# Optimization experiments

Measured on AMD Instinct MI355X. Metric: run time of the kernel, lower is better.

## Reference

```python
import jax, jax.numpy as jnp
import numpy as np

S, B, D_MODEL, H, DH = 2048, 2, 1024, 16, 64
FACTOR = 1.0 / np.sqrt(DH).astype(np.float32)


def setup_inputs() -> dict:
    key = jax.random.key(0)
    ks = jax.random.split(key, 12)
    sc = 0.02
    inp = {
        'query': jax.random.normal(ks[0], (S, B, D_MODEL), jnp.float32),
        'key': jax.random.normal(ks[1], (S, B, D_MODEL), jnp.float32),
        'value': jax.random.normal(ks[2], (S, B, D_MODEL), jnp.float32),
        # causal mask [seq_q, seq_k, 1]; 0 -> masked
        'mask': jnp.tril(jnp.ones((S, S), dtype=bool))[:, :, None],
        'Wq': jax.random.normal(ks[3], (H * DH, D_MODEL), jnp.float32) * sc,
        'bq': jnp.zeros((H * DH,), jnp.float32),
        'Wk': jax.random.normal(ks[4], (H * DH, D_MODEL), jnp.float32) * sc,
        'bk': jnp.zeros((H * DH,), jnp.float32),
        'Wv': jax.random.normal(ks[5], (H * DH, D_MODEL), jnp.float32) * sc,
        'bv': jnp.zeros((H * DH,), jnp.float32),
        'Wo': jax.random.normal(ks[6], (D_MODEL, H * DH), jnp.float32) * sc,
        'bo': jnp.zeros((D_MODEL,), jnp.float32),
    }
    return inp


def _split_heads(x):
    # pattern: 's b (head_dim head_num) -> s b head_num head_dim' (head_dim is OUTER)
    s, b, _ = x.shape
    return x.reshape(s, b, DH, H).transpose(0, 1, 3, 2)  # [s,b,H,DH]


def reference(query, key, value, mask, Wq, bq, Wk, bk, Wv, bv, Wo, bo):
    q = _split_heads(query @ Wq.T + bq)
    k = _split_heads(key @ Wk.T + bk)
    v = _split_heads(value @ Wv.T + bv)
    scores = jnp.einsum('ibhd,jbhd->ijbh', q, k) * FACTOR  # [i,j,b,h]
    scores = jnp.where(mask[..., None], scores, -jnp.inf)
    attn = jax.nn.softmax(scores, axis=1)  # softmax over keys (dim=1)
    out = jnp.einsum('ijbh,jbhd->ibhd', attn, v)  # [i,b,h,d]
    out = out.reshape(S, B, H * DH)  # 'i b h d -> i b (h d)'
    return out @ Wo.T + bo
```

## Files before the change

kernel.cpp:

```cpp
#include <hip/hip_runtime.h>


typedef float f32x4 __attribute__((ext_vector_type(4)));
typedef float f32x16 __attribute__((ext_vector_type(16)));
typedef __bf16 bf16x8_t __attribute__((ext_vector_type(8)));
typedef unsigned short ushort8 __attribute__((ext_vector_type(8)));
typedef unsigned int uint4v __attribute__((ext_vector_type(4)));
typedef unsigned int uint2v __attribute__((ext_vector_type(2)));

#define S_LEN 2048
#define BATCH 2
#define DMODEL 1024
#define NHEAD 16
#define DHEAD 64
#define K_SCALE 0.18033688011112042f

__device__ __forceinline__ unsigned short f2bf(float x) {
  unsigned int u = __builtin_bit_cast(unsigned int, x);
  u += 0x7fffu + ((u >> 16) & 1u);
  return (unsigned short)(u >> 16);
}

__device__ __forceinline__ f32x4 mfma16(ushort8 a, ushort8 b, f32x4 c) {
  return __builtin_amdgcn_mfma_f32_16x16x32_bf16(
      __builtin_bit_cast(bf16x8_t, a), __builtin_bit_cast(bf16x8_t, b), c, 0, 0, 0);
}
__device__ __forceinline__ f32x16 mfma32(ushort8 a, ushort8 b, f32x16 c) {
  return __builtin_amdgcn_mfma_f32_32x32x16_bf16(
      __builtin_bit_cast(bf16x8_t, a), __builtin_bit_cast(bf16x8_t, b), c, 0, 0, 0);
}

__device__ __forceinline__ ushort8 pack8(float4 a, float4 b, float s) {
  ushort8 t;
  t[0] = f2bf(a.x * s); t[1] = f2bf(a.y * s); t[2] = f2bf(a.z * s); t[3] = f2bf(a.w * s);
  t[4] = f2bf(b.x * s); t[5] = f2bf(b.y * s); t[6] = f2bf(b.z * s); t[7] = f2bf(b.w * s);
  return t;
}

__device__ __forceinline__ void gload16(unsigned short* lds, const unsigned short* g) {
  __builtin_amdgcn_global_load_lds(
      (const __attribute__((address_space(1))) unsigned int*)g,
      (__attribute__((address_space(3))) unsigned int*)lds, 16, 0, 0);
}

__global__ __launch_bounds__(256) void cvt_kernel(
    const float* __restrict__ q, const float* __restrict__ k, const float* __restrict__ v,
    const float* __restrict__ wq, const float* __restrict__ wk,
    const float* __restrict__ wv, const float* __restrict__ wo,
    unsigned short* __restrict__ qB, unsigned short* __restrict__ kB,
    unsigned short* __restrict__ vB, unsigned short* __restrict__ wqB,
    unsigned short* __restrict__ wkB, unsigned short* __restrict__ wvB,
    unsigned short* __restrict__ woB)
{
  const int c = blockIdx.x * 256 + threadIdx.x;
  const float* s; unsigned short* d; int base;
  if      (c < 524288)  { s = q;  d = qB;  base = 0; }
  else if (c < 1048576) { s = k;  d = kB;  base = 524288; }
  else if (c < 1572864) { s = v;  d = vB;  base = 1048576; }
  else if (c < 1703936) { s = wq; d = wqB; base = 1572864; }
  else if (c < 1835008) { s = wk; d = wkB; base = 1703936; }
  else if (c < 1966080) { s = wv; d = wvB; base = 1835008; }
  else                  { s = wo; d = woB; base = 1966080; }
  const size_t off = (size_t)(c - base) * 8;
  const float4 v0 = *reinterpret_cast<const float4*>(s + off);
  const float4 v1 = *reinterpret_cast<const float4*>(s + off + 4);
  *reinterpret_cast<ushort8*>(d + off) = pack8(v0, v1, 1.0f);
}

template<bool OUTBF16>
__global__ __launch_bounds__(256) void gemm_bf16_kernel(
    const unsigned short* __restrict__ A, const unsigned short* __restrict__ W,
    const float* __restrict__ bias, void* __restrict__ Cv, float oscale)
{
  __shared__ __align__(16) unsigned short As[2][128 * 64];
  __shared__ __align__(16) unsigned short Ws[2][64 * 64];
  const int tid = threadIdx.x;
  const int lane = tid & 63;
  const int w = tid >> 6;
  const int wm = (w >> 1) * 64, wn = (w & 1) * 32;
  const int g = lane >> 4, lr = lane & 15;

  const int bid = (int)blockIdx.x;
  const int widx = (bid & 7) * 64 + (bid >> 3);
  const int n0 = (widx & 15) * 64;
  const int m0 = (widx >> 4) * 128;

  f32x4 acc[4][2] = {};

#define STAGE(buf, k0)                                                              \
  {                                                                                 \
    _Pragma("unroll")                                                               \
    for (int ii = 0; ii < 4; ++ii) {                                                \
      const int c = ii * 256 + tid;                                                 \
      const int row = c >> 3;                                                       \
      const int sl = (c & 7) ^ (row & 7);                                           \
      gload16(&As[buf][c * 8], A + (size_t)(m0 + row) * DMODEL + (k0) + sl * 8);    \
    }                                                                               \
    _Pragma("unroll")                                                               \
    for (int ii = 0; ii < 2; ++ii) {                                                \
      const int c = ii * 256 + tid;                                                 \
      const int row = c >> 3;                                                       \
      const int sl = (c & 7) ^ (row & 7);                                           \
      gload16(&Ws[buf][c * 8], W + (size_t)(n0 + row) * DMODEL + (k0) + sl * 8);    \
    }                                                                               \
  }

  STAGE(0, 0);
  int cur = 0;

  for (int t = 0; t < 16; ++t) {
    __syncthreads();
    if (t < 15) STAGE(cur ^ 1, (t + 1) * 64);

    const char* ab = (const char*)&As[cur][0];
    const char* wb = (const char*)&Ws[cur][0];
#pragma unroll
    for (int kk = 0; kk < 2; ++kk) {
      ushort8 af[4], bw[2];
#pragma unroll
      for (int mt = 0; mt < 4; ++mt) {
        const int row = wm + mt * 16 + lr;
        af[mt] = *reinterpret_cast<const ushort8*>(
            ab + row * 128 + (((kk * 4 + g) ^ (row & 7)) << 4));
      }
#pragma unroll
      for (int nt = 0; nt < 2; ++nt) {
        const int row = wn + nt * 16 + lr;
        bw[nt] = *reinterpret_cast<const ushort8*>(
            wb + row * 128 + (((kk * 4 + g) ^ (row & 7)) << 4));
      }
      __builtin_amdgcn_s_setprio(1);
#pragma unroll
      for (int mt = 0; mt < 4; ++mt)
#pragma unroll
        for (int nt = 0; nt < 2; ++nt)
          acc[mt][nt] = mfma16(af[mt], bw[nt], acc[mt][nt]);
      __builtin_amdgcn_s_setprio(0);
    }
    cur ^= 1;
  }
#undef STAGE

#pragma unroll
  for (int nt = 0; nt < 2; ++nt) {
    const int col = n0 + wn + nt * 16 + lr;
    const float bv = bias[col];
#pragma unroll
    for (int mt = 0; mt < 4; ++mt)
#pragma unroll
      for (int r = 0; r < 4; ++r) {
        const int rowg = m0 + wm + mt * 16 + g * 4 + r;
        const float vv = (acc[mt][nt][r] + bv) * oscale;
        if constexpr (OUTBF16)
          ((unsigned short*)Cv)[(size_t)rowg * DMODEL + col] = f2bf(vv);
        else
          ((float*)Cv)[(size_t)rowg * DMODEL + col] = vv;
      }
  }
}

__global__ __launch_bounds__(256) void head_tr0_kernel(
    const unsigned short* __restrict__ in, unsigned short* __restrict__ out)
{
  __shared__ __align__(16) unsigned short T[32 * 256];
  const int tid = threadIdx.x;
  const int n0 = blockIdx.x * 32, o0 = blockIdx.y * 256;
#pragma unroll
  for (int i = 0; i < 4; ++i) {
    const int c = i * 256 + tid;
    const int row = c >> 5, c8 = c & 31;
    ushort8 v = *reinterpret_cast<const ushort8*>(in + (size_t)(n0 + row) * DMODEL + o0 + c8 * 8);
    int y = (row * 512 + c8 * 16) ^ ((row & 3) << 5);
    *reinterpret_cast<ushort8*>((char*)T + y) = v;
  }
  __syncthreads();
  const int d0 = o0 >> 4, s0 = n0 >> 1;
#pragma unroll
  for (int rep = 0; rep < 2; ++rep) {
    const int e = rep * 256 + tid;
    const int hh = e & 15, s = (e >> 4) & 15, b = (e >> 8) & 1;
    const int n = s * 2 + b;
    unsigned short vals[16];
#pragma unroll
    for (int dd = 0; dd < 16; ++dd) {
      int y = n * 512 + ((dd * 32 + hh * 2) ^ ((n & 3) << 5));
      vals[dd] = *(const unsigned short*)((const char*)T + y);
    }
    uint4v w0, w1;
#pragma unroll
    for (int j = 0; j < 4; ++j) {
      w0[j] = (unsigned)vals[2 * j] | ((unsigned)vals[2 * j + 1] << 16);
      w1[j] = (unsigned)vals[8 + 2 * j] | ((unsigned)vals[8 + 2 * j + 1] << 16);
    }
    unsigned short* dst = out + ((size_t)(b * 16 + hh) * S_LEN + s0 + s) * DHEAD + d0;
    *reinterpret_cast<uint4v*>(dst) = w0;
    *reinterpret_cast<uint4v*>(dst + 8) = w1;
  }
}

__global__ __launch_bounds__(256) void head_tr1_kernel(
    const unsigned short* __restrict__ in, unsigned short* __restrict__ out)
{
  __shared__ __align__(16) unsigned short T[64 * 64];
  const int tid = threadIdx.x;
  const int n0 = blockIdx.x * 64, o0 = blockIdx.y * 64;
#pragma unroll
  for (int i = 0; i < 2; ++i) {
    const int c = i * 256 + tid;
    const int row = c >> 3, c8 = c & 7;
    ushort8 v = *reinterpret_cast<const ushort8*>(in + (size_t)(n0 + row) * DMODEL + o0 + c8 * 8);
    int y = (row * 128 + c8 * 16) ^ ((row & 7) << 4);
    *reinterpret_cast<ushort8*>((char*)T + y) = v;
  }
  __syncthreads();
  const int d0 = o0 >> 4, s0 = n0 >> 1;
  const int shalf = tid & 1, seg = tid >> 1;
  const int dd = seg & 3, hh = (seg >> 2) & 15, b = (seg >> 6) & 1;
  unsigned short vals[16];
#pragma unroll
  for (int i = 0; i < 16; ++i) {
    const int s = shalf * 16 + i;
    const int n = s * 2 + b;
    int y = n * 128 + (((dd * 16 + hh) * 2) ^ ((n & 7) << 4));
    vals[i] = *(const unsigned short*)((const char*)T + y);
  }
  uint4v w0, w1;
#pragma unroll
  for (int j = 0; j < 4; ++j) {
    w0[j] = (unsigned)vals[2 * j] | ((unsigned)vals[2 * j + 1] << 16);
    w1[j] = (unsigned)vals[8 + 2 * j] | ((unsigned)vals[8 + 2 * j + 1] << 16);
  }
  unsigned short* dst = out + ((size_t)(b * 16 + hh) * DHEAD + d0 + dd) * S_LEN + s0 + shalf * 16;
  *reinterpret_cast<uint4v*>(dst) = w0;
  *reinterpret_cast<uint4v*>(dst + 8) = w1;
}

__global__ __launch_bounds__(256, 2) void attn_kernel(
    const unsigned short* __restrict__ Qh, const unsigned short* __restrict__ Kh,
    const unsigned short* __restrict__ Vh, unsigned short* __restrict__ O)
{
  __shared__ __align__(16) unsigned short Ks[2][64 * 64];
  __shared__ __align__(16) unsigned short Vs[2][64 * 64];

  const int tid = threadIdx.x;
  const int lane = tid & 63;
  const int w = tid >> 6;
  const int ln31 = lane & 31;
  const int hf = lane >> 5;

  const int bx = blockIdx.x;
  const int hb = bx & 31;
  const int head = hb & 15, b = hb >> 4;
  const int i = bx >> 5;
  const int qt = (i < 8) ? (15 - i) : (i - 8);
  const int q0 = qt * 128;
  const size_t hoff = (size_t)(b * NHEAD + head) * (S_LEN * DHEAD);
  const unsigned short* Qg = Qh + hoff;
  const unsigned short* Kg = Kh + hoff;
  const unsigned short* Vg = Vh + hoff;

  ushort8 qf[4];
  {
    const int qrow = q0 + w * 32 + ln31;
#pragma unroll
    for (int kt = 0; kt < 4; ++kt)
      qf[kt] = *reinterpret_cast<const ushort8*>(Qg + (size_t)qrow * DHEAD + kt * 16 + hf * 8);
  }

  f32x16 oa0 = {0}, oa1 = {0};
  float mrun = -1e30f, ssum = 0.f;

  const int nkt = 2 * qt + 2;
  const int qg = q0 + w * 32 + ln31;
  const int qw_max = q0 + w * 32 + 31;

  ushort8 sK0, sK1, sV0, sV1;
  const int r0 = tid >> 3, f0 = tid & 7;
  const int r1 = r0 + 32, f1 = f0;

#define LOAD_TILES(kv)                                                            \
  {                                                                               \
    sK0 = *reinterpret_cast<const ushort8*>(Kg + (size_t)((kv) + r0) * 64 + f0 * 8); \
    sK1 = *reinterpret_cast<const ushort8*>(Kg + (size_t)((kv) + r1) * 64 + f1 * 8); \
    sV0 = *reinterpret_cast<const ushort8*>(Vg + (size_t)r0 * S_LEN + (kv) + f0 * 8); \
    sV1 = *reinterpret_cast<const ushort8*>(Vg + (size_t)r1 * S_LEN + (kv) + f1 * 8); \
  }
#define WRITE_TILES(buf)                                                          \
  {                                                                               \
    *reinterpret_cast<ushort8*>((char*)&Ks[buf][0] + ((r0 * 128 + f0 * 16) ^ ((r0 & 7) << 4))) = sK0; \
    *reinterpret_cast<ushort8*>((char*)&Ks[buf][0] + ((r1 * 128 + f1 * 16) ^ ((r1 & 7) << 4))) = sK1; \
    *reinterpret_cast<ushort8*>((char*)&Vs[buf][0] + ((r0 * 128 + f0 * 16) ^ ((r0 & 7) << 4))) = sV0; \
    *reinterpret_cast<ushort8*>((char*)&Vs[buf][0] + ((r1 * 128 + f1 * 16) ^ ((r1 & 7) << 4))) = sV1; \
  }

  LOAD_TILES(0);
  WRITE_TILES(0);
  __syncthreads();
  int cur = 0;

  const int kb0 = ln31 * 128 + ((hf * 16) ^ ((ln31 & 7) << 4));
  const int kb1 = (32 + ln31) * 128 + ((hf * 16) ^ (((32 + ln31) & 7) << 4));

  for (int t = 0; t < nkt; ++t) {
    const int kv0 = t * 64;
    const bool has_next = (t + 1) < nkt;
    if (has_next) LOAD_TILES(kv0 + 64);

    if (kv0 <= qw_max) {
      f32x16 sc0 = {0}, sc1 = {0};
      {
        const char* ksb = (const char*)&Ks[cur][0];
        __builtin_amdgcn_s_setprio(1);
#pragma unroll
        for (int kt = 0; kt < 4; ++kt) {
          ushort8 kf0 = *reinterpret_cast<const ushort8*>(ksb + (kb0 ^ (kt << 5)));
          ushort8 kf1 = *reinterpret_cast<const ushort8*>(ksb + (kb1 ^ (kt << 5)));
          sc0 = mfma32(kf0, qf[kt], sc0);
          sc1 = mfma32(kf1, qf[kt], sc1);
        }
        __builtin_amdgcn_s_setprio(0);
      }

      if (has_next) WRITE_TILES(cur ^ 1);

      if (kv0 + 63 > q0 + w * 32) {
#pragma unroll
        for (int r = 0; r < 16; ++r) {
          const int keyb = kv0 + (r & 3) + 8 * (r >> 2) + 4 * hf;
          if (keyb > qg) sc0[r] = -1e30f;
          if (keyb + 32 > qg) sc1[r] = -1e30f;
        }
      }

      float pmax = sc0[0];
#pragma unroll
      for (int r = 1; r < 16; ++r) pmax = fmaxf(pmax, sc0[r]);
#pragma unroll
      for (int r = 0; r < 16; ++r) pmax = fmaxf(pmax, sc1[r]);
      pmax = fmaxf(pmax, __shfl_xor(pmax, 32, 64));

      if (!__all(pmax <= mrun + 8.0f)) {
        const float mnew = fmaxf(mrun, pmax);
        const float scl = exp2f(mrun - mnew);
        ssum *= scl;
#pragma unroll
        for (int r = 0; r < 16; ++r) { oa0[r] *= scl; oa1[r] *= scl; }
        mrun = mnew;
      }

      float pv0[16], pv1[16];
      float psum = 0.f;
#pragma unroll
      for (int r = 0; r < 16; ++r) {
        pv0[r] = exp2f(sc0[r] - mrun);
        pv1[r] = exp2f(sc1[r] - mrun);
        psum += pv0[r] + pv1[r];
      }
      psum += __shfl_xor(psum, 32, 64);
      ssum += psum;

      unsigned int cc[16], pc[16];
#pragma unroll
      for (int j = 0; j < 8; ++j) {
        asm("v_cvt_pk_bf16_f32 %0, %1, %2" : "=v"(cc[j]) : "v"(pv0[2 * j]), "v"(pv0[2 * j + 1]));
        asm("v_cvt_pk_bf16_f32 %0, %1, %2" : "=v"(cc[8 + j]) : "v"(pv1[2 * j]), "v"(pv1[2 * j + 1]));
      }
#pragma unroll
      for (int j = 0; j < 16; ++j)
        pc[j] = (unsigned int)__shfl_xor((int)cc[j], 32, 64);

      uint4v pfw[4];
#pragma unroll
      for (int mt = 0; mt < 2; ++mt) {
#pragma unroll
        for (int ktl = 0; ktl < 2; ++ktl) {
          const int o = mt * 8 + ktl * 4;
          uint4v u;
          u[0] = hf ? pc[o + 2] : cc[o + 0];
          u[1] = hf ? pc[o + 3] : cc[o + 1];
          u[2] = hf ? cc[o + 2] : pc[o + 0];
          u[3] = hf ? cc[o + 3] : pc[o + 1];
          pfw[mt * 2 + ktl] = u;
        }
      }

      {
        const char* vsb = (const char*)&Vs[cur][0];
        __builtin_amdgcn_s_setprio(1);
#pragma unroll
        for (int kt = 0; kt < 4; ++kt) {
          ushort8 vf0 = *reinterpret_cast<const ushort8*>(vsb + (kb0 ^ (kt << 5)));
          ushort8 vf1 = *reinterpret_cast<const ushort8*>(vsb + (kb1 ^ (kt << 5)));
          ushort8 pfr = __builtin_bit_cast(ushort8, pfw[kt]);
          oa0 = mfma32(vf0, pfr, oa0);
          oa1 = mfma32(vf1, pfr, oa1);
        }
        __builtin_amdgcn_s_setprio(0);
      }
    } else {
      if (has_next) WRITE_TILES(cur ^ 1);
    }

    __syncthreads();
    cur ^= 1;
  }

  const float inv = 1.0f / ssum;
  unsigned short* ob = O + ((size_t)qg * BATCH + b) * DMODEL + head * DHEAD;
#pragma unroll
  for (int mt2 = 0; mt2 < 2; ++mt2) {
#pragma unroll
    for (int rq = 0; rq < 4; ++rq) {
      const int dd = mt2 * 32 + 8 * rq + 4 * hf;
      const f32x16& a = mt2 ? oa1 : oa0;
      unsigned int w0, w1;
      asm("v_cvt_pk_bf16_f32 %0, %1, %2" : "=v"(w0)
          : "v"(a[4 * rq + 0] * inv), "v"(a[4 * rq + 1] * inv));
      asm("v_cvt_pk_bf16_f32 %0, %1, %2" : "=v"(w1)
          : "v"(a[4 * rq + 2] * inv), "v"(a[4 * rq + 3] * inv));
      uint2v pk = { w0, w1 };
      *reinterpret_cast<uint2v*>(ob + dd) = pk;
    }
  }
#undef LOAD_TILES
#undef WRITE_TILES
}

extern "C" void kernel_launch(void* const* d_in, const int* in_sizes, int n_in,
                              void* d_out, int out_size, void* d_ws, size_t ws_size,
                              hipStream_t stream)
{
  (void)in_sizes; (void)n_in; (void)out_size; (void)ws_size;
  const float* query = (const float*)d_in[0];
  const float* key_  = (const float*)d_in[1];
  const float* value = (const float*)d_in[2];
  const float* Wq = (const float*)d_in[4];
  const float* bq = (const float*)d_in[5];
  const float* Wk = (const float*)d_in[6];
  const float* bk = (const float*)d_in[7];
  const float* Wv = (const float*)d_in[8];
  const float* bv = (const float*)d_in[9];
  const float* Wo = (const float*)d_in[10];
  const float* bo = (const float*)d_in[11];
  float* out = (float*)d_out;

  const size_t NE = (size_t)4096 * DMODEL;
  const size_t NW = (size_t)DMODEL * DMODEL;
  unsigned short* qB  = (unsigned short*)d_ws;
  unsigned short* kB  = qB + NE;
  unsigned short* vB  = kB + NE;
  unsigned short* g1  = vB + NE;
  unsigned short* Qh  = g1 + NE;
  unsigned short* Kh  = Qh + NE;
  unsigned short* Vh  = Kh + NE;
  unsigned short* wqB = Vh + NE;
  unsigned short* wkB = wqB + NW;
  unsigned short* wvB = wkB + NW;
  unsigned short* woB = wvB + NW;
  unsigned short* aO  = qB;

  dim3 t0grid(128, 4);
  dim3 t1grid(64, 16);

  cvt_kernel<<<dim3(8192), 256, 0, stream>>>(query, key_, value, Wq, Wk, Wv, Wo,
                                             qB, kB, vB, wqB, wkB, wvB, woB);
  gemm_bf16_kernel<true><<<dim3(512), 256, 0, stream>>>(qB, wqB, bq, g1, 1.0f);
  head_tr0_kernel<<<t0grid, 256, 0, stream>>>(g1, Qh);
  gemm_bf16_kernel<true><<<dim3(512), 256, 0, stream>>>(kB, wkB, bk, g1, K_SCALE);
  head_tr0_kernel<<<t0grid, 256, 0, stream>>>(g1, Kh);
  gemm_bf16_kernel<true><<<dim3(512), 256, 0, stream>>>(vB, wvB, bv, g1, 1.0f);
  head_tr1_kernel<<<t1grid, 256, 0, stream>>>(g1, Vh);
  attn_kernel<<<dim3(512), 256, 0, stream>>>(Qh, Kh, Vh, aO);
  gemm_bf16_kernel<false><<<dim3(512), 256, 0, stream>>>(aO, woB, bo, out, 1.0f);
}
```

Baseline: 155.1 us.

## Use direct global-to-LDS async loads with 64-row query tiles in attention

The attention kernel now runs 1024 blocks of 128 threads, each owning 64 query rows, in place of 512 blocks of 256 threads owning 128 rows. Launch bounds change to allow three blocks per CU. K/V staging switches from register round-trips to direct global-to-LDS loads (gload16), with the XOR swizzle applied to the source addresses. The loop is reordered so the barrier sits first and the next tile is prefetched before compute. Masking is limited to the last tile, and the per-warp causal skip branch is gone. The intent is finer causal load balance and better overlap of loads with MFMA work. The cost is that K/V tiles are fetched twice as often per query row.

```diff
diff --git a/kernel.cpp b/kernel.cpp
--- a/kernel.cpp
+++ b/kernel.cpp
@@ -235,7 +235,7 @@
   *reinterpret_cast<uint4v*>(dst + 8) = w1;
 }
 
-__global__ __launch_bounds__(256, 2) void attn_kernel(
+__global__ __launch_bounds__(128, 3) void attn_kernel(
     const unsigned short* __restrict__ Qh, const unsigned short* __restrict__ Kh,
     const unsigned short* __restrict__ Vh, unsigned short* __restrict__ O)
 {
@@ -251,9 +251,9 @@
   const int bx = blockIdx.x;
   const int hb = bx & 31;
   const int head = hb & 15, b = hb >> 4;
-  const int i = bx >> 5;
-  const int qt = (i < 8) ? (15 - i) : (i - 8);
-  const int q0 = qt * 128;
+  const int qt = 31 - (bx >> 5);
+  const int q0 = qt * 64;
+  const int nkt = qt + 1;
   const size_t hoff = (size_t)(b * NHEAD + head) * (S_LEN * DHEAD);
   const unsigned short* Qg = Qh + hoff;
   const unsigned short* Kg = Kh + hoff;
@@ -269,141 +269,129 @@
 
   f32x16 oa0 = {0}, oa1 = {0};
   float mrun = -1e30f, ssum = 0.f;
-
-  const int nkt = 2 * qt + 2;
   const int qg = q0 + w * 32 + ln31;
-  const int qw_max = q0 + w * 32 + 31;
-
-  ushort8 sK0, sK1, sV0, sV1;
-  const int r0 = tid >> 3, f0 = tid & 7;
-  const int r1 = r0 + 32, f1 = f0;
-
-#define LOAD_TILES(kv)                                                            \
-  {                                                                               \
-    sK0 = *reinterpret_cast<const ushort8*>(Kg + (size_t)((kv) + r0) * 64 + f0 * 8); \
-    sK1 = *reinterpret_cast<const ushort8*>(Kg + (size_t)((kv) + r1) * 64 + f1 * 8); \
-    sV0 = *reinterpret_cast<const ushort8*>(Vg + (size_t)r0 * S_LEN + (kv) + f0 * 8); \
-    sV1 = *reinterpret_cast<const ushort8*>(Vg + (size_t)r1 * S_LEN + (kv) + f1 * 8); \
-  }
-#define WRITE_TILES(buf)                                                          \
-  {                                                                               \
-    *reinterpret_cast<ushort8*>((char*)&Ks[buf][0] + ((r0 * 128 + f0 * 16) ^ ((r0 & 7) << 4))) = sK0; \
-    *reinterpret_cast<ushort8*>((char*)&Ks[buf][0] + ((r1 * 128 + f1 * 16) ^ ((r1 & 7) << 4))) = sK1; \
-    *reinterpret_cast<ushort8*>((char*)&Vs[buf][0] + ((r0 * 128 + f0 * 16) ^ ((r0 & 7) << 4))) = sV0; \
-    *reinterpret_cast<ushort8*>((char*)&Vs[buf][0] + ((r1 * 128 + f1 * 16) ^ ((r1 & 7) << 4))) = sV1; \
-  }
-
-  LOAD_TILES(0);
-  WRITE_TILES(0);
-  __syncthreads();
+
+#define STAGE(buf, kv)                                                             \
+  {                                                                                \
+    _Pragma("unroll")                                                              \
+    for (int ii = 0; ii < 4; ++ii) {                                               \
+      const int c = ii * 128 + tid;                                                \
+      const int row = c >> 3;                                                      \
+      const int sl = (c & 7) ^ (row & 7);                                          \
+      gload16(&Ks[buf][c * 8], Kg + (size_t)((kv) + row) * 64 + sl * 8);           \
+    }                                                                              \
+    _Pragma("unroll")                                                              \
+    for (int ii = 0; ii < 4; ++ii) {                                               \
+      const int c = ii * 128 + tid;                                                \
+      const int row = c >> 3;                                                      \
+      const int sl = (c & 7) ^ (row & 7);                                          \
+      gload16(&Vs[buf][c * 8], Vg + (size_t)row * S_LEN + (kv) + sl * 8);          \
+    }                                                                              \
+  }
+
+  STAGE(0, 0);
   int cur = 0;
 
   const int kb0 = ln31 * 128 + ((hf * 16) ^ ((ln31 & 7) << 4));
-  const int kb1 = (32 + ln31) * 128 + ((hf * 16) ^ (((32 + ln31) & 7) << 4));
+  const int kb1 = (32 + ln31) * 128 + ((hf * 16) ^ ((ln31 & 7) << 4));
 
   for (int t = 0; t < nkt; ++t) {
     const int kv0 = t * 64;
-    const bool has_next = (t + 1) < nkt;
-    if (has_next) LOAD_TILES(kv0 + 64);
-
-    if (kv0 <= qw_max) {
-      f32x16 sc0 = {0}, sc1 = {0};
-      {
-        const char* ksb = (const char*)&Ks[cur][0];
-        __builtin_amdgcn_s_setprio(1);
-#pragma unroll
-        for (int kt = 0; kt < 4; ++kt) {
-          ushort8 kf0 = *reinterpret_cast<const ushort8*>(ksb + (kb0 ^ (kt << 5)));
-          ushort8 kf1 = *reinterpret_cast<const ushort8*>(ksb + (kb1 ^ (kt << 5)));
-          sc0 = mfma32(kf0, qf[kt], sc0);
-          sc1 = mfma32(kf1, qf[kt], sc1);
-        }
-        __builtin_amdgcn_s_setprio(0);
-      }
-
-      if (has_next) WRITE_TILES(cur ^ 1);
-
-      if (kv0 + 63 > q0 + w * 32) {
-#pragma unroll
-        for (int r = 0; r < 16; ++r) {
-          const int keyb = kv0 + (r & 3) + 8 * (r >> 2) + 4 * hf;
-          if (keyb > qg) sc0[r] = -1e30f;
-          if (keyb + 32 > qg) sc1[r] = -1e30f;
-        }
-      }
-
-      float pmax = sc0[0];
-#pragma unroll
-      for (int r = 1; r < 16; ++r) pmax = fmaxf(pmax, sc0[r]);
-#pragma unroll
-      for (int r = 0; r < 16; ++r) pmax = fmaxf(pmax, sc1[r]);
-      pmax = fmaxf(pmax, __shfl_xor(pmax, 32, 64));
-
-      if (!__all(pmax <= mrun + 8.0f)) {
-        const float mnew = fmaxf(mrun, pmax);
-        const float scl = exp2f(mrun - mnew);
-        ssum *= scl;
-#pragma unroll
-        for (int r = 0; r < 16; ++r) { oa0[r] *= scl; oa1[r] *= scl; }
-        mrun = mnew;
-      }
-
-      float pv0[16], pv1[16];
-      float psum = 0.f;
+    __syncthreads();
+    if (t + 1 < nkt) STAGE(cur ^ 1, kv0 + 64);
+
+    f32x16 sc0 = {0}, sc1 = {0};
+    {
+      const char* ksb = (const char*)&Ks[cur][0];
+      __builtin_amdgcn_s_setprio(1);
+#pragma unroll
+      for (int kt = 0; kt < 4; ++kt) {
+        ushort8 kf0 = *reinterpret_cast<const ushort8*>(ksb + (kb0 ^ (kt << 5)));
+        ushort8 kf1 = *reinterpret_cast<const ushort8*>(ksb + (kb1 ^ (kt << 5)));
+        sc0 = mfma32(kf0, qf[kt], sc0);
+        sc1 = mfma32(kf1, qf[kt], sc1);
+      }
+      __builtin_amdgcn_s_setprio(0);
+    }
+
+    if (t == nkt - 1) {
 #pragma unroll
       for (int r = 0; r < 16; ++r) {
-        pv0[r] = exp2f(sc0[r] - mrun);
-        pv1[r] = exp2f(sc1[r] - mrun);
-        psum += pv0[r] + pv1[r];
-      }
-      psum += __shfl_xor(psum, 32, 64);
-      ssum += psum;
-
-      unsigned int cc[16], pc[16];
-#pragma unroll
-      for (int j = 0; j < 8; ++j) {
-        asm("v_cvt_pk_bf16_f32 %0, %1, %2" : "=v"(cc[j]) : "v"(pv0[2 * j]), "v"(pv0[2 * j + 1]));
-        asm("v_cvt_pk_bf16_f32 %0, %1, %2" : "=v"(cc[8 + j]) : "v"(pv1[2 * j]), "v"(pv1[2 * j + 1]));
-      }
-#pragma unroll
-      for (int j = 0; j < 16; ++j)
-        pc[j] = (unsigned int)__shfl_xor((int)cc[j], 32, 64);
-
-      uint4v pfw[4];
-#pragma unroll
-      for (int mt = 0; mt < 2; ++mt) {
-#pragma unroll
-        for (int ktl = 0; ktl < 2; ++ktl) {
-          const int o = mt * 8 + ktl * 4;
-          uint4v u;
-          u[0] = hf ? pc[o + 2] : cc[o + 0];
-          u[1] = hf ? pc[o + 3] : cc[o + 1];
-          u[2] = hf ? cc[o + 2] : pc[o + 0];
-          u[3] = hf ? cc[o + 3] : pc[o + 1];
-          pfw[mt * 2 + ktl] = u;
-        }
-      }
-
-      {
-        const char* vsb = (const char*)&Vs[cur][0];
-        __builtin_amdgcn_s_setprio(1);
-#pragma unroll
-        for (int kt = 0; kt < 4; ++kt) {
-          ushort8 vf0 = *reinterpret_cast<const ushort8*>(vsb + (kb0 ^ (kt << 5)));
-          ushort8 vf1 = *reinterpret_cast<const ushort8*>(vsb + (kb1 ^ (kt << 5)));
-          ushort8 pfr = __builtin_bit_cast(ushort8, pfw[kt]);
-          oa0 = mfma32(vf0, pfr, oa0);
-          oa1 = mfma32(vf1, pfr, oa1);
-        }
-        __builtin_amdgcn_s_setprio(0);
-      }
-    } else {
-      if (has_next) WRITE_TILES(cur ^ 1);
-    }
-
-    __syncthreads();
+        const int keyb = kv0 + (r & 3) + 8 * (r >> 2) + 4 * hf;
+        if (keyb > qg) sc0[r] = -1e30f;
+        if (keyb + 32 > qg) sc1[r] = -1e30f;
+      }
+    }
+
+    float pmax = sc0[0];
+#pragma unroll
+    for (int r = 1; r < 16; ++r) pmax = fmaxf(pmax, sc0[r]);
+#pragma unroll
+    for (int r = 0; r < 16; ++r) pmax = fmaxf(pmax, sc1[r]);
+    pmax = fmaxf(pmax, __shfl_xor(pmax, 32, 64));
+
+    if (!__all(pmax <= mrun + 8.0f)) {
+      const float mnew = fmaxf(mrun, pmax);
+      const float scl = exp2f(mrun - mnew);
+      ssum *= scl;
+#pragma unroll
+      for (int r = 0; r < 16; ++r) { oa0[r] *= scl; oa1[r] *= scl; }
+      mrun = mnew;
+    }
+
+    float pv0[16], pv1[16];
+    float psum = 0.f;
+#pragma unroll
+    for (int r = 0; r < 16; ++r) {
+      pv0[r] = exp2f(sc0[r] - mrun);
+      pv1[r] = exp2f(sc1[r] - mrun);
+      psum += pv0[r] + pv1[r];
+    }
+    psum += __shfl_xor(psum, 32, 64);
+    ssum += psum;
+
+    unsigned int cc[16], pc[16];
+#pragma unroll
+    for (int j = 0; j < 8; ++j) {
+      asm("v_cvt_pk_bf16_f32 %0, %1, %2" : "=v"(cc[j]) : "v"(pv0[2 * j]), "v"(pv0[2 * j + 1]));
+      asm("v_cvt_pk_bf16_f32 %0, %1, %2" : "=v"(cc[8 + j]) : "v"(pv1[2 * j]), "v"(pv1[2 * j + 1]));
+    }
+#pragma unroll
+    for (int j = 0; j < 16; ++j)
+      pc[j] = (unsigned int)__shfl_xor((int)cc[j], 32, 64);
+
+    uint4v pfw[4];
+#pragma unroll
+    for (int mt = 0; mt < 2; ++mt) {
+#pragma unroll
+      for (int ktl = 0; ktl < 2; ++ktl) {
+        const int o = mt * 8 + ktl * 4;
+        uint4v u;
+        u[0] = hf ? pc[o + 2] : cc[o + 0];
+        u[1] = hf ? pc[o + 3] : cc[o + 1];
+        u[2] = hf ? cc[o + 2] : pc[o + 0];
+        u[3] = hf ? cc[o + 3] : pc[o + 1];
+        pfw[mt * 2 + ktl] = u;
+      }
+    }
+
+    {
+      const char* vsb = (const char*)&Vs[cur][0];
+      __builtin_amdgcn_s_setprio(1);
+#pragma unroll
+      for (int kt = 0; kt < 4; ++kt) {
+        ushort8 vf0 = *reinterpret_cast<const ushort8*>(vsb + (kb0 ^ (kt << 5)));
+        ushort8 vf1 = *reinterpret_cast<const ushort8*>(vsb + (kb1 ^ (kt << 5)));
+        ushort8 pfr = __builtin_bit_cast(ushort8, pfw[kt]);
+        oa0 = mfma32(vf0, pfr, oa0);
+        oa1 = mfma32(vf1, pfr, oa1);
+      }
+      __builtin_amdgcn_s_setprio(0);
+    }
+
     cur ^= 1;
   }
+#undef STAGE
 
   const float inv = 1.0f / ssum;
   unsigned short* ob = O + ((size_t)qg * BATCH + b) * DMODEL + head * DHEAD;
@@ -422,8 +410,6 @@
       *reinterpret_cast<uint2v*>(ob + dd) = pk;
     }
   }
-#undef LOAD_TILES
-#undef WRITE_TILES
 }
 
 extern "C" void kernel_launch(void* const* d_in, const int* in_sizes, int n_in,
@@ -470,6 +456,6 @@
   head_tr0_kernel<<<t0grid, 256, 0, stream>>>(g1, Kh);
   gemm_bf16_kernel<true><<<dim3(512), 256, 0, stream>>>(vB, wvB, bv, g1, 1.0f);
   head_tr1_kernel<<<t1grid, 256, 0, stream>>>(g1, Vh);
-  attn_kernel<<<dim3(512), 256, 0, stream>>>(Qh, Kh, Vh, aO);
+  attn_kernel<<<dim3(1024), 128, 0, stream>>>(Qh, Kh, Vh, aO);
   gemm_bf16_kernel<false><<<dim3(512), 256, 0, stream>>>(aO, woB, bo, out, 1.0f);
 }
```

Measured after the change: 156.1 us. No clear change (+0.6%).
